# Kernel tuning notes

Measured on AMD Instinct MI355X. Metric: run time of the kernel, lower is better.

The kernel has to match this reference:

```python
import jax, jax.numpy as jnp
import numpy as np

B, N, L, S, H, E, D = 4, 7, 512, 512, 8, 64, 64

def setup_inputs() -> dict:
    key = jax.random.key(0)
    kq, kk, kv = jax.random.split(key, 3)
    queries = jax.random.normal(kq, (B, N, L, H, E), dtype=jnp.float32)
    keys = jax.random.normal(kk, (B, N, S, H, E), dtype=jnp.float32)
    values = jax.random.normal(kv, (B, N, S, H, D), dtype=jnp.float32)
    return {"queries": queries, "keys": keys, "values": values}

def reference(queries, keys, values):
    # queries: [B,N,L,H,E], keys: [B,N,S,H,E], values: [B,N,S,H,D]
    E_ = queries.shape[-1]
    scale = 1.0 / jnp.sqrt(jnp.asarray(E_, dtype=queries.dtype))
    # scores: [B,N,H,L,S]
    scores = jnp.einsum('bnlhe,bnshe->bnhls', queries, keys)
    attn = jax.nn.softmax(scale * scores, axis=-1)  # dropout p=0 (eval)
    V = jnp.einsum('bnhls,bnshd->bnlhd', attn, values)
    return V
```

## Files before the change

kernel.cpp:

```cpp
#include <hip/hip_runtime.h>

#define B_ 4
#define N_ 7
#define L_ 512
#define S_ 512
#define H_ 8
#define E_ 64
#define D_ 64

constexpr int QT  = 128;
constexpr int ST  = 128;
constexpr int NT  = S_ / ST;
constexpr int KP  = 72;
constexpr int VPW = 65;

typedef _Float16 f16x8 __attribute__((ext_vector_type(8)));
typedef _Float16 f16x4 __attribute__((ext_vector_type(4)));
typedef float    f32x4 __attribute__((ext_vector_type(4)));

#if __has_builtin(__builtin_amdgcn_exp2f)
#define EXP2F __builtin_amdgcn_exp2f
#else
#define EXP2F exp2f
#endif

#if __has_builtin(__builtin_amdgcn_cvt_pkrtz)
__device__ __forceinline__ f16x4 pack4(float a, float b, float c, float d) {
    union { unsigned u[2]; f16x4 h; } cv;
    auto lo = __builtin_amdgcn_cvt_pkrtz(a, b);
    auto hi = __builtin_amdgcn_cvt_pkrtz(c, d);
    __builtin_memcpy(&cv.u[0], &lo, 4);
    __builtin_memcpy(&cv.u[1], &hi, 4);
    return cv.h;
}
#else
__device__ __forceinline__ f16x4 pack4(float a, float b, float c, float d) {
    f16x4 w; w[0]=(_Float16)a; w[1]=(_Float16)b; w[2]=(_Float16)c; w[3]=(_Float16)d;
    return w;
}
#endif

__global__ __launch_bounds__(512, 4)
void attn_fwd(const float* __restrict__ Q, const float* __restrict__ K,
              const float* __restrict__ V, float* __restrict__ O)
{
    __shared__ _Float16 Ks[ST * KP];
    __shared__ unsigned Vw[D_ * VPW];
    _Float16* Vh = (_Float16*)Vw;

    const int bnh   = blockIdx.x;
    const int h     = bnh & (H_ - 1);
    const int bn    = bnh >> 3;
    const int qbase = blockIdx.y * QT;

    const int tid  = threadIdx.x;
    const int wid  = tid >> 6;
    const int lane = tid & 63;
    const int quad = lane >> 4;
    const int m16  = lane & 15;

    const size_t row = H_ * E_;
    const float* Qp = Q + ((size_t)bn * L_ * H_ + h) * E_;
    const float* Kp = K + ((size_t)bn * S_ * H_ + h) * E_;
    const float* Vp = V + ((size_t)bn * S_ * H_ + h) * D_;
    float*       Op = O + ((size_t)bn * L_ * H_ + h) * D_;

    const int sr = tid >> 4;
    const int sc = (tid & 15) * 4;

    const float qsc = 0.125f * 1.4426950408889634f;
    f16x8 qf[2];
    #pragma unroll
    for (int kt = 0; kt < 2; ++kt) {
        const float* p = Qp + (size_t)(qbase + wid*16 + m16) * row + kt*32 + quad*8;
        float4 a = *(const float4*)p;
        float4 b = *(const float4*)(p + 4);
        f16x8 f;
        f[0]=(_Float16)(a.x*qsc); f[1]=(_Float16)(a.y*qsc);
        f[2]=(_Float16)(a.z*qsc); f[3]=(_Float16)(a.w*qsc);
        f[4]=(_Float16)(b.x*qsc); f[5]=(_Float16)(b.y*qsc);
        f[6]=(_Float16)(b.z*qsc); f[7]=(_Float16)(b.w*qsc);
        qf[kt] = f;
    }

    const f32x4 fzero = {0.f, 0.f, 0.f, 0.f};
    f32x4 of[4];
    #pragma unroll
    for (int dt = 0; dt < 4; ++dt) of[dt] = fzero;
    float l_run = 0.f;

    float4 k0 = *(const float4*)(Kp + (size_t)(sr     ) * row + sc);
    float4 k1 = *(const float4*)(Kp + (size_t)(sr + 32) * row + sc);
    float4 k2 = *(const float4*)(Kp + (size_t)(sr + 64) * row + sc);
    float4 k3 = *(const float4*)(Kp + (size_t)(sr + 96) * row + sc);
    float4 v0 = *(const float4*)(Vp + (size_t)(sr     ) * row + sc);
    float4 v1 = *(const float4*)(Vp + (size_t)(sr + 32) * row + sc);
    float4 v2 = *(const float4*)(Vp + (size_t)(sr + 64) * row + sc);
    float4 v3 = *(const float4*)(Vp + (size_t)(sr + 96) * row + sc);

    for (int it = 0; it < NT; ++it) {
        #define STK(kv, R) *(f16x4*)&Ks[(R)*KP + sc] = pack4(kv.x, kv.y, kv.z, kv.w);
        STK(k0, sr) STK(k1, sr + 32) STK(k2, sr + 64) STK(k3, sr + 96)
        #undef STK
        #define STV(vv, R) { \
            Vh[(sc+0)*130 + (R)] = (_Float16)vv.x; \
            Vh[(sc+1)*130 + (R)] = (_Float16)vv.y; \
            Vh[(sc+2)*130 + (R)] = (_Float16)vv.z; \
            Vh[(sc+3)*130 + (R)] = (_Float16)vv.w; }
        STV(v0, sr) STV(v1, sr + 32) STV(v2, sr + 64) STV(v3, sr + 96)
        #undef STV
        __syncthreads();

        if (it + 1 < NT) {
            const float* kp2 = Kp + (size_t)((it + 1) * ST) * row;
            const float* vp2 = Vp + (size_t)((it + 1) * ST) * row;
            k0 = *(const float4*)(kp2 + (size_t)(sr     ) * row + sc);
            k1 = *(const float4*)(kp2 + (size_t)(sr + 32) * row + sc);
            k2 = *(const float4*)(kp2 + (size_t)(sr + 64) * row + sc);
            k3 = *(const float4*)(kp2 + (size_t)(sr + 96) * row + sc);
            v0 = *(const float4*)(vp2 + (size_t)(sr     ) * row + sc);
            v1 = *(const float4*)(vp2 + (size_t)(sr + 32) * row + sc);
            v2 = *(const float4*)(vp2 + (size_t)(sr + 64) * row + sc);
            v3 = *(const float4*)(vp2 + (size_t)(sr + 96) * row + sc);
        }

        f32x4 acc[8];
        #pragma unroll
        for (int st = 0; st < 8; ++st) acc[st] = fzero;
        #pragma unroll
        for (int st = 0; st < 8; ++st) {
            #pragma unroll
            for (int kt = 0; kt < 2; ++kt) {
                f16x8 kf = *(const f16x8*)&Ks[(st*16 + m16)*KP + kt*32 + quad*8];
                acc[st] = __builtin_amdgcn_mfma_f32_16x16x32_f16(kf, qf[kt], acc[st], 0,0,0);
            }
        }

        float rsum = 0.f;
        #pragma unroll
        for (int st = 0; st < 8; ++st)
            #pragma unroll
            for (int r = 0; r < 4; ++r) {
                float p = EXP2F(acc[st][r]);
                acc[st][r] = p;
                rsum += p;
            }
        rsum += __shfl_xor(rsum, 16);
        rsum += __shfl_xor(rsum, 32);
        l_run += rsum;

        #pragma unroll
        for (int st = 0; st < 8; ++st) {
            f16x4 pf = pack4(acc[st][0], acc[st][1], acc[st][2], acc[st][3]);
            #pragma unroll
            for (int dt = 0; dt < 4; ++dt) {
                int d  = dt*16 + m16;
                int wi = VPW*d + 8*st + 2*quad;
                unsigned w0 = Vw[wi], w1 = Vw[wi + 1];
                union { unsigned u[2]; f16x4 h; } cv;
                cv.u[0] = w0; cv.u[1] = w1;
                of[dt] = __builtin_amdgcn_mfma_f32_16x16x16f16(pf, cv.h, of[dt], 0,0,0);
            }
        }

        __syncthreads();
    }

    #pragma unroll
    for (int r = 0; r < 4; ++r) {
        float inv = 1.0f / __shfl(l_run, quad*4 + r);
        float* op = Op + (size_t)(qbase + wid*16 + quad*4 + r) * row + m16;
        #pragma unroll
        for (int dt = 0; dt < 4; ++dt)
            op[dt*16] = of[dt][r] * inv;
    }
}

extern "C" void kernel_launch(void* const* d_in, const int* in_sizes, int n_in,
                              void* d_out, int out_size, void* d_ws, size_t ws_size,
                              hipStream_t stream)
{
    const float* Q = (const float*)d_in[0];
    const float* K = (const float*)d_in[1];
    const float* V = (const float*)d_in[2];
    float* O = (float*)d_out;
    dim3 grid(B_ * N_ * H_, L_ / QT);
    attn_fwd<<<grid, 512, 0, stream>>>(Q, K, V, O);
}
```

Before: 139.4 us.

## Use 256-thread blocks with 32 query rows per wave and double-buffered 64-row K/V tiles

Halves the block size so each wave handles two 16-row query tiles. Each K and V fragment read from shared memory then feeds two MFMAs, which cuts LDS traffic per FLOP. K/V tiles shrink to 64 rows and are double-buffered in shared memory, so the trailing __syncthreads per iteration can be dropped. V is now stored transposed as packed half2 words with a new padding, which replaces the scattered 16-bit stores with 32-bit ones. The cost is more registers per thread (two output accumulators and two Q fragment sets) and twice as many loop iterations.

Measured after the change: 184.6 us. +32.4%, slower.

```diff
diff --git a/kernel.cpp b/kernel.cpp
--- a/kernel.cpp
+++ b/kernel.cpp
@@ -9,10 +9,10 @@
 #define D_ 64
 
 constexpr int QT  = 128;
-constexpr int ST  = 128;
+constexpr int ST  = 64;
 constexpr int NT  = S_ / ST;
 constexpr int KP  = 72;
-constexpr int VPW = 65;
+constexpr int VP2 = 17;
 
 typedef _Float16 f16x8 __attribute__((ext_vector_type(8)));
 typedef _Float16 f16x4 __attribute__((ext_vector_type(4)));
@@ -40,13 +40,18 @@
 }
 #endif
 
-__global__ __launch_bounds__(512, 4)
+__device__ __forceinline__ unsigned pack2r(float a, float b) {
+    union { _Float16 h[2]; unsigned u; } cv;
+    cv.h[0] = (_Float16)a; cv.h[1] = (_Float16)b;
+    return cv.u;
+}
+
+__global__ __launch_bounds__(256, 4)
 void attn_fwd(const float* __restrict__ Q, const float* __restrict__ K,
               const float* __restrict__ V, float* __restrict__ O)
 {
-    __shared__ _Float16 Ks[ST * KP];
-    __shared__ unsigned Vw[D_ * VPW];
-    _Float16* Vh = (_Float16*)Vw;
+    __shared__ _Float16 Ks[2][ST * KP];
+    __shared__ uint2    Vd[2][D_ * VP2];
 
     const int bnh   = blockIdx.x;
     const int h     = bnh & (H_ - 1);
@@ -67,112 +72,121 @@
 
     const int sr = tid >> 4;
     const int sc = (tid & 15) * 4;
+    const int s0 = (tid & 31) * 2;
+    const int d0 = (tid >> 5) * 8;
 
     const float qsc = 0.125f * 1.4426950408889634f;
-    f16x8 qf[2];
+    f16x8 qf[2][2];
     #pragma unroll
-    for (int kt = 0; kt < 2; ++kt) {
-        const float* p = Qp + (size_t)(qbase + wid*16 + m16) * row + kt*32 + quad*8;
-        float4 a = *(const float4*)p;
-        float4 b = *(const float4*)(p + 4);
-        f16x8 f;
-        f[0]=(_Float16)(a.x*qsc); f[1]=(_Float16)(a.y*qsc);
-        f[2]=(_Float16)(a.z*qsc); f[3]=(_Float16)(a.w*qsc);
-        f[4]=(_Float16)(b.x*qsc); f[5]=(_Float16)(b.y*qsc);
-        f[6]=(_Float16)(b.z*qsc); f[7]=(_Float16)(b.w*qsc);
-        qf[kt] = f;
+    for (int q = 0; q < 2; ++q) {
+        #pragma unroll
+        for (int kt = 0; kt < 2; ++kt) {
+            const float* p = Qp + (size_t)(qbase + wid*32 + q*16 + m16) * row + kt*32 + quad*8;
+            float4 a = *(const float4*)p;
+            float4 b = *(const float4*)(p + 4);
+            f16x8 f;
+            f[0]=(_Float16)(a.x*qsc); f[1]=(_Float16)(a.y*qsc);
+            f[2]=(_Float16)(a.z*qsc); f[3]=(_Float16)(a.w*qsc);
+            f[4]=(_Float16)(b.x*qsc); f[5]=(_Float16)(b.y*qsc);
+            f[6]=(_Float16)(b.z*qsc); f[7]=(_Float16)(b.w*qsc);
+            qf[q][kt] = f;
+        }
     }
 
     const f32x4 fzero = {0.f, 0.f, 0.f, 0.f};
-    f32x4 of[4];
+    f32x4 of[2][4];
     #pragma unroll
-    for (int dt = 0; dt < 4; ++dt) of[dt] = fzero;
-    float l_run = 0.f;
-
-    float4 k0 = *(const float4*)(Kp + (size_t)(sr     ) * row + sc);
-    float4 k1 = *(const float4*)(Kp + (size_t)(sr + 32) * row + sc);
-    float4 k2 = *(const float4*)(Kp + (size_t)(sr + 64) * row + sc);
-    float4 k3 = *(const float4*)(Kp + (size_t)(sr + 96) * row + sc);
-    float4 v0 = *(const float4*)(Vp + (size_t)(sr     ) * row + sc);
-    float4 v1 = *(const float4*)(Vp + (size_t)(sr + 32) * row + sc);
-    float4 v2 = *(const float4*)(Vp + (size_t)(sr + 64) * row + sc);
-    float4 v3 = *(const float4*)(Vp + (size_t)(sr + 96) * row + sc);
-
+    for (int q = 0; q < 2; ++q)
+        #pragma unroll
+        for (int dt = 0; dt < 4; ++dt) of[q][dt] = fzero;
+    float l_run0 = 0.f, l_run1 = 0.f;
+
+    float4 k0  = *(const float4*)(Kp + (size_t)(sr     ) * row + sc);
+    float4 k1  = *(const float4*)(Kp + (size_t)(sr + 16) * row + sc);
+    float4 k2  = *(const float4*)(Kp + (size_t)(sr + 32) * row + sc);
+    float4 k3  = *(const float4*)(Kp + (size_t)(sr + 48) * row + sc);
+    float4 vA0 = *(const float4*)(Vp + (size_t)(s0    ) * row + d0);
+    float4 vA1 = *(const float4*)(Vp + (size_t)(s0    ) * row + d0 + 4);
+    float4 vB0 = *(const float4*)(Vp + (size_t)(s0 + 1) * row + d0);
+    float4 vB1 = *(const float4*)(Vp + (size_t)(s0 + 1) * row + d0 + 4);
+
+    #pragma unroll 2
     for (int it = 0; it < NT; ++it) {
-        #define STK(kv, R) *(f16x4*)&Ks[(R)*KP + sc] = pack4(kv.x, kv.y, kv.z, kv.w);
-        STK(k0, sr) STK(k1, sr + 32) STK(k2, sr + 64) STK(k3, sr + 96)
-        #undef STK
-        #define STV(vv, R) { \
-            Vh[(sc+0)*130 + (R)] = (_Float16)vv.x; \
-            Vh[(sc+1)*130 + (R)] = (_Float16)vv.y; \
-            Vh[(sc+2)*130 + (R)] = (_Float16)vv.z; \
-            Vh[(sc+3)*130 + (R)] = (_Float16)vv.w; }
-        STV(v0, sr) STV(v1, sr + 32) STV(v2, sr + 64) STV(v3, sr + 96)
-        #undef STV
+        const int p = it & 1;
+
+        *(f16x4*)&Ks[p][(sr     )*KP + sc] = pack4(k0.x, k0.y, k0.z, k0.w);
+        *(f16x4*)&Ks[p][(sr + 16)*KP + sc] = pack4(k1.x, k1.y, k1.z, k1.w);
+        *(f16x4*)&Ks[p][(sr + 32)*KP + sc] = pack4(k2.x, k2.y, k2.z, k2.w);
+        *(f16x4*)&Ks[p][(sr + 48)*KP + sc] = pack4(k3.x, k3.y, k3.z, k3.w);
+        {
+            unsigned* vw = (unsigned*)&Vd[p][0];
+            const int vb = s0 >> 1;
+            vw[(d0+0)*(2*VP2) + vb] = pack2r(vA0.x, vB0.x);
+            vw[(d0+1)*(2*VP2) + vb] = pack2r(vA0.y, vB0.y);
+            vw[(d0+2)*(2*VP2) + vb] = pack2r(vA0.z, vB0.z);
+            vw[(d0+3)*(2*VP2) + vb] = pack2r(vA0.w, vB0.w);
+            vw[(d0+4)*(2*VP2) + vb] = pack2r(vA1.x, vB1.x);
+            vw[(d0+5)*(2*VP2) + vb] = pack2r(vA1.y, vB1.y);
+            vw[(d0+6)*(2*VP2) + vb] = pack2r(vA1.z, vB1.z);
+            vw[(d0+7)*(2*VP2) + vb] = pack2r(vA1.w, vB1.w);
+        }
         __syncthreads();
 
         if (it + 1 < NT) {
             const float* kp2 = Kp + (size_t)((it + 1) * ST) * row;
             const float* vp2 = Vp + (size_t)((it + 1) * ST) * row;
-            k0 = *(const float4*)(kp2 + (size_t)(sr     ) * row + sc);
-            k1 = *(const float4*)(kp2 + (size_t)(sr + 32) * row + sc);
-            k2 = *(const float4*)(kp2 + (size_t)(sr + 64) * row + sc);
-            k3 = *(const float4*)(kp2 + (size_t)(sr + 96) * row + sc);
-            v0 = *(const float4*)(vp2 + (size_t)(sr     ) * row + sc);
-            v1 = *(const float4*)(vp2 + (size_t)(sr + 32) * row + sc);
-            v2 = *(const float4*)(vp2 + (size_t)(sr + 64) * row + sc);
-            v3 = *(const float4*)(vp2 + (size_t)(sr + 96) * row + sc);
-        }
-
-        f32x4 acc[8];
-        #pragma unroll
-        for (int st = 0; st < 8; ++st) acc[st] = fzero;
-        #pragma unroll
-        for (int st = 0; st < 8; ++st) {
-            #pragma unroll
-            for (int kt = 0; kt < 2; ++kt) {
-                f16x8 kf = *(const f16x8*)&Ks[(st*16 + m16)*KP + kt*32 + quad*8];
-                acc[st] = __builtin_amdgcn_mfma_f32_16x16x32_f16(kf, qf[kt], acc[st], 0,0,0);
-            }
-        }
-
-        float rsum = 0.f;
-        #pragma unroll
-        for (int st = 0; st < 8; ++st)
-            #pragma unroll
-            for (int r = 0; r < 4; ++r) {
-                float p = EXP2F(acc[st][r]);
-                acc[st][r] = p;
-                rsum += p;
-            }
-        rsum += __shfl_xor(rsum, 16);
-        rsum += __shfl_xor(rsum, 32);
-        l_run += rsum;
-
-        #pragma unroll
-        for (int st = 0; st < 8; ++st) {
-            f16x4 pf = pack4(acc[st][0], acc[st][1], acc[st][2], acc[st][3]);
+            k0  = *(const float4*)(kp2 + (size_t)(sr     ) * row + sc);
+            k1  = *(const float4*)(kp2 + (size_t)(sr + 16) * row + sc);
+            k2  = *(const float4*)(kp2 + (size_t)(sr + 32) * row + sc);
+            k3  = *(const float4*)(kp2 + (size_t)(sr + 48) * row + sc);
+            vA0 = *(const float4*)(vp2 + (size_t)(s0    ) * row + d0);
+            vA1 = *(const float4*)(vp2 + (size_t)(s0    ) * row + d0 + 4);
+            vB0 = *(const float4*)(vp2 + (size_t)(s0 + 1) * row + d0);
+            vB1 = *(const float4*)(vp2 + (size_t)(s0 + 1) * row + d0 + 4);
+        }
+
+        const _Float16* ks = Ks[p];
+        const uint2*    vd = Vd[p];
+        #pragma unroll
+        for (int st = 0; st < 4; ++st) {
+            const f16x8 kf0 = *(const f16x8*)&ks[(st*16 + m16)*KP +      quad*8];
+            const f16x8 kf1 = *(const f16x8*)&ks[(st*16 + m16)*KP + 32 + quad*8];
+            f32x4 a0 = fzero, a1 = fzero;
+            a0 = __builtin_amdgcn_mfma_f32_16x16x32_f16(kf0, qf[0][0], a0, 0,0,0);
+            a0 = __builtin_amdgcn_mfma_f32_16x16x32_f16(kf1, qf[0][1], a0, 0,0,0);
+            a1 = __builtin_amdgcn_mfma_f32_16x16x32_f16(kf0, qf[1][0], a1, 0,0,0);
+            a1 = __builtin_amdgcn_mfma_f32_16x16x32_f16(kf1, qf[1][1], a1, 0,0,0);
+
+            float e00 = EXP2F(a0[0]), e01 = EXP2F(a0[1]), e02 = EXP2F(a0[2]), e03 = EXP2F(a0[3]);
+            float e10 = EXP2F(a1[0]), e11 = EXP2F(a1[1]), e12 = EXP2F(a1[2]), e13 = EXP2F(a1[3]);
+            l_run0 += (e00 + e01) + (e02 + e03);
+            l_run1 += (e10 + e11) + (e12 + e13);
+            f16x4 pf0 = pack4(e00, e01, e02, e03);
+            f16x4 pf1 = pack4(e10, e11, e12, e13);
+
             #pragma unroll
             for (int dt = 0; dt < 4; ++dt) {
-                int d  = dt*16 + m16;
-                int wi = VPW*d + 8*st + 2*quad;
-                unsigned w0 = Vw[wi], w1 = Vw[wi + 1];
-                union { unsigned u[2]; f16x4 h; } cv;
-                cv.u[0] = w0; cv.u[1] = w1;
-                of[dt] = __builtin_amdgcn_mfma_f32_16x16x16f16(pf, cv.h, of[dt], 0,0,0);
+                union { uint2 u; f16x4 h; } cv;
+                cv.u = vd[(dt*16 + m16)*VP2 + st*4 + quad];
+                of[0][dt] = __builtin_amdgcn_mfma_f32_16x16x16f16(pf0, cv.h, of[0][dt], 0,0,0);
+                of[1][dt] = __builtin_amdgcn_mfma_f32_16x16x16f16(pf1, cv.h, of[1][dt], 0,0,0);
             }
         }
-
-        __syncthreads();
     }
 
     #pragma unroll
-    for (int r = 0; r < 4; ++r) {
-        float inv = 1.0f / __shfl(l_run, quad*4 + r);
-        float* op = Op + (size_t)(qbase + wid*16 + quad*4 + r) * row + m16;
-        #pragma unroll
-        for (int dt = 0; dt < 4; ++dt)
-            op[dt*16] = of[dt][r] * inv;
+    for (int q = 0; q < 2; ++q) {
+        float lr = q ? l_run1 : l_run0;
+        lr += __shfl_xor(lr, 16);
+        lr += __shfl_xor(lr, 32);
+        #pragma unroll
+        for (int r = 0; r < 4; ++r) {
+            float inv = 1.0f / __shfl(lr, quad*4 + r);
+            float* op = Op + (size_t)(qbase + wid*32 + q*16 + quad*4 + r) * row + m16;
+            #pragma unroll
+            for (int dt = 0; dt < 4; ++dt)
+                op[dt*16] = of[q][dt][r] * inv;
+        }
     }
 }
 
@@ -185,5 +199,5 @@
     const float* V = (const float*)d_in[2];
     float* O = (float*)d_out;
     dim3 grid(B_ * N_ * H_, L_ / QT);
-    attn_fwd<<<grid, 512, 0, stream>>>(Q, K, V, O);
-}
+    attn_fwd<<<grid, 256, 0, stream>>>(Q, K, V, O);
+}
```
